# Performance work log

Measured on AMD Instinct MI355X. Metric: run time of the kernel, lower is better.

## Reference

```python
import jax, jax.numpy as jnp
import numpy as np

B, CIN, CE, CA, N, S = 2, 64, 128, 128, 1024, 32
SCALE = np.sqrt(np.float32(CA))  # scale_mode == 'dimfts'


def _vnlin(W, x):
    # VNLinear: linear map over the channel dim of (B, C, 3, N, S)
    return jnp.einsum('oc,bcdns->bodns', W, x)


def setup_inputs() -> dict:
    key = jax.random.key(0)
    ks = jax.random.split(key, 16)
    def w(k, o, i):
        return (jax.random.normal(k, (o, i), jnp.float32) / np.sqrt(np.float32(i)))
    return {
        'group_xyz': jax.random.normal(ks[0], (B, N, S, 3), jnp.float32),
        'group_fts': jax.random.normal(ks[1], (B, CIN, 3, N, S), jnp.float32),
        'query_xyz': jax.random.normal(ks[2], (B, N, 3), jnp.float32),
        'W_e1': w(ks[3], CE, CIN), 'W_e2': w(ks[4], CE, CE),
        'W_q': w(ks[5], CA, CE), 'W_k': w(ks[6], CA, CE), 'W_v': w(ks[7], CA, CE),
        'W_r1': w(ks[8], 64, 1), 'W_r2': w(ks[9], CA, 64),
        'W_std': w(ks[10], 3, CA),
        'W_f1': w(ks[11], CA, CA * 3), 'b_f1': jax.random.normal(ks[12], (CA,), jnp.float32) * 0.02,
        'W_f2': w(ks[13], CA, CA), 'b_f2': jax.random.normal(ks[14], (CA,), jnp.float32) * 0.02,
    }


def reference(group_xyz, group_fts, query_xyz, W_e1, W_e2, W_q, W_k, W_v,
              W_r1, W_r2, W_std, W_f1, b_f1, W_f2, b_f2):
    # vnn_e: two stacked VNLinear layers
    group_emb = _vnlin(W_e2, _vnlin(W_e1, group_fts))        # (B, CE, 3, N, S)
    query_emb = group_emb[..., :1]                           # (B, CE, 3, N, 1)
    q = _vnlin(W_q, query_emb)                               # (B, CA, 3, N, 1)
    k = _vnlin(W_k, group_emb)                               # (B, CA, 3, N, S)
    v = _vnlin(W_v, group_emb)                               # (B, CA, 3, N, S)

    # positional relation: xyz_rel -> (B, 1, 3, N, S) -> vnn_r
    xyz_rel = group_xyz - query_xyz[:, :, None, :]           # (B, N, S, 3)
    xyz_rel = jnp.transpose(xyz_rel[:, :, :, None, :], (0, 3, 4, 1, 2))  # (B,1,3,N,S)
    pos_rel = _vnlin(W_r2, _vnlin(W_r1, xyz_rel))            # (B, CA, 3, N, S)

    # relation_func == 'sub'
    attn = q - k + pos_rel                                   # (B, CA, 3, N, S)

    # VNStdFeatureLin (dim=5, no frame normalization): z0 = VNLinear(CA->3)
    z0 = _vnlin(W_std, attn)                                 # (B, 3, 3, N, S)
    attn = jnp.einsum('bijns,bjkns->bikns', attn, z0)        # (B, CA, 3, N, S) invariant

    # attn_fwd: 1x1 conv -> ReLU -> 1x1 conv on (B, CA*3, N, S)
    attn = attn.reshape(B, CA * 3, N, S)
    h = jax.nn.relu(jnp.einsum('oc,bcns->bons', W_f1, attn) + b_f1[:, None, None])
    a = jnp.einsum('oc,bcns->bons', W_f2, h) + b_f2[:, None, None]  # (B, CA, N, S)

    a = jax.nn.softmax(a[:, :, None, :, :] / SCALE, axis=-1)  # (B, CA, 1, N, S)
    v = v + pos_rel
    resi = jnp.sum(a * v, axis=-1)                            # (B, CA, 3, N)
    return resi
```

## Files before the change

kernel.cpp:

```cpp
#include <hip/hip_runtime.h>
#include <hip/hip_bf16.h>
#include <math.h>

typedef __hip_bfloat16  bf16;
typedef __hip_bfloat162 bf162;
typedef __attribute__((ext_vector_type(8))) short short8;
typedef __attribute__((ext_vector_type(4))) float f32x4;

#define BB   2
#define CINC 64
#define NN   1024
#define SSS  32
#define NS   (NN * SSS)

#define OFF_WE21 0
#define OFF_WR   8192
#define OFF_KBA  8320
#define OFF_VB   16512
#define OFF_F1B  20608
#define OFF_F2B  45184
#define WS_NEED_FLOATS 53376

#define S_ATT_B  0
#define S_FTS_B  26112
#define S_SCR_B  26112
#define S_XYZ_B  30720
#define SMEM_BYTES 30912

__device__ __forceinline__ float bf2f(short s) {
    unsigned int u = ((unsigned int)(unsigned short)s) << 16;
    return __uint_as_float(u);
}
__device__ __forceinline__ short f2bf(float f) {
    bf16 h = __float2bfloat16(f);
    return *reinterpret_cast<short*>(&h);
}
__device__ __forceinline__ unsigned pk2(float a, float b) {
    bf162 p = __float22bfloat162_rn(make_float2(a, b));
    return *reinterpret_cast<unsigned*>(&p);
}

__global__ __launch_bounds__(256) void prep1(const float* __restrict__ We1,
                                             const float* __restrict__ We2,
                                             float* __restrict__ ws) {
    int e = blockIdx.x * 256 + threadIdx.x;
    int o = e >> 6, c = e & 63;
    float acc = 0.f;
    for (int m = 0; m < 128; ++m)
        acc = fmaf(We2[o * 128 + m], We1[m * 64 + c], acc);
    ws[OFF_WE21 + o * 64 + c] = acc;
}

__global__ __launch_bounds__(256) void prep2(const float* __restrict__ Wq,
                                             const float* __restrict__ Wk,
                                             const float* __restrict__ Wv,
                                             const float* __restrict__ Wr1,
                                             const float* __restrict__ Wr2,
                                             const float* __restrict__ Wf1,
                                             const float* __restrict__ Wf2,
                                             float* __restrict__ ws) {
    const float* we21 = ws + OFF_WE21;
    int e = blockIdx.x * 256 + threadIdx.x;
    if (e < 16384) {
        int i = e >> 7, c2 = e & 127;
        const float* W = (c2 < 64) ? Wk : Wq;
        int c = c2 & 63;
        float acc = 0.f;
        for (int o = 0; o < 128; ++o)
            acc = fmaf(W[i * 128 + o], we21[o * 64 + c], acc);
        if (c2 >= 64) acc = -acc;
        ((bf16*)(ws + OFF_KBA))[i * 128 + c2] = __float2bfloat16(acc);
    } else if (e < 24576) {
        int le = e - 16384;
        int i = le >> 6, c = le & 63;
        float acc = 0.f;
        for (int o = 0; o < 128; ++o)
            acc = fmaf(Wv[i * 128 + o], we21[o * 64 + c], acc);
        ((bf16*)(ws + OFF_VB))[i * 64 + c] = __float2bfloat16(acc);
    } else if (e < 24704) {
        int i = e - 24576;
        float acc = 0.f;
        for (int m = 0; m < 64; ++m)
            acc = fmaf(Wr2[i * 64 + m], Wr1[m], acc);
        ws[OFF_WR + i] = acc;
    } else if (e < 24704 + 49152) {
        int f = e - 24704;
        int o = f / 384, kp = f - o * 384;
        int c = (kp & 127) * 3 + (kp >> 7);
        ((bf16*)(ws + OFF_F1B))[f] = __float2bfloat16(Wf1[o * 384 + c]);
    } else if (e < 24704 + 49152 + 16384) {
        int f = e - (24704 + 49152);
        ((bf16*)(ws + OFF_F2B))[f] = __float2bfloat16(Wf2[f]);
    }
}

__global__ __launch_bounds__(256, 2) void fused_main(
        const float* __restrict__ gxyz, const float* __restrict__ gfts,
        const float* __restrict__ qxyz, const float* __restrict__ Wstd,
        const float* __restrict__ bf1,  const float* __restrict__ bf2,
        const float* __restrict__ ws,   float* __restrict__ out) {
    extern __shared__ char smc[];
    short* s_att  = (short*)(smc + S_ATT_B);
    short* h_t    = s_att;
    short* a_t    = s_att + 4352;
    short* fts_s  = (short*)(smc + S_FTS_B);
    float* s_scr  = (float*)(smc + S_SCR_B);
    short* s_xyzh = (short*)(smc + S_XYZ_B);

    const int t    = threadIdx.x;
    const int bid  = blockIdx.x;
    const int b    = bid >> 10;
    const int n    = bid & 1023;
    const int w    = t >> 6;
    const int lane = t & 63;
    const int quad = lane >> 4;
    const int lq   = lane & 15;
    const int wb   = 32 * w;

    const float* gb = gfts + (size_t)b * (CINC * 3 * NS) + n * SSS;

    short8 Ka[2][4], Va[2][2];
    {
        const short* kba = (const short*)(ws + OFF_KBA);
        const short* vbb = (const short*)(ws + OFF_VB);
        #pragma unroll
        for (int it = 0; it < 2; ++it) {
            int i = wb + it * 16 + lq;
            #pragma unroll
            for (int kc = 0; kc < 4; ++kc)
                Ka[it][kc] = *(const short8*)(kba + i * 128 + kc * 32 + quad * 8);
            #pragma unroll
            for (int kc = 0; kc < 2; ++kc)
                Va[it][kc] = *(const short8*)(vbb + i * 64 + kc * 32 + quad * 8);
        }
    }
    float wr2[2] = { ws[OFF_WR + wb + lq], ws[OFF_WR + wb + 16 + lq] };

    uint2 va_pk[6][2];
    #pragma unroll
    for (int h = 0; h < 3; ++h) {
        {
            int cp = t >> 3;
            int ml = (t & 7) * 4;
            const float* fb = gb + (2 * cp * 3 + h) * NS + ml;
            float4 f0 = *(const float4*)(fb);
            float4 f1 = *(const float4*)(fb + 3 * NS);
            short* dst = fts_s + ml * 72 + 2 * cp;
            *(unsigned*)(dst)       = pk2(f0.x, f1.x);
            *(unsigned*)(dst + 72)  = pk2(f0.y, f1.y);
            *(unsigned*)(dst + 144) = pk2(f0.z, f1.z);
            *(unsigned*)(dst + 216) = pk2(f0.w, f1.w);
        }
        if (h == 0 && t >= 160) {
            int id = t - 160;
            int d = id >> 5, s = id & 31;
            s_xyzh[id] = f2bf(gxyz[((b * NN + n) * SSS + s) * 3 + d]
                              - qxyz[(b * NN + n) * 3 + d]);
        }
        __syncthreads();

        const short* qp = fts_s + quad * 8;
        short8 aq0 = *(const short8*)(qp);
        short8 aq1 = *(const short8*)(qp + 32);
        #pragma unroll
        for (int mt_h = 0; mt_h < 2; ++mt_h) {
            int mt = h * 2 + mt_h;
            const short* ap = fts_s + (mt_h * 16 + lq) * 72 + quad * 8;
            short8 a0 = *(const short8*)(ap);
            short8 a1 = *(const short8*)(ap + 32);
            #pragma unroll
            for (int it = 0; it < 2; ++it) {
                f32x4 kk = {0.f, 0.f, 0.f, 0.f};
                kk = __builtin_amdgcn_mfma_f32_16x16x32_bf16(a0,  Ka[it][0], kk, 0, 0, 0);
                kk = __builtin_amdgcn_mfma_f32_16x16x32_bf16(a1,  Ka[it][1], kk, 0, 0, 0);
                kk = __builtin_amdgcn_mfma_f32_16x16x32_bf16(aq0, Ka[it][2], kk, 0, 0, 0);
                kk = __builtin_amdgcn_mfma_f32_16x16x32_bf16(aq1, Ka[it][3], kk, 0, 0, 0);
                f32x4 vv = {0.f, 0.f, 0.f, 0.f};
                vv = __builtin_amdgcn_mfma_f32_16x16x32_bf16(a0,  Va[it][0], vv, 0, 0, 0);
                vv = __builtin_amdgcn_mfma_f32_16x16x32_bf16(a1,  Va[it][1], vv, 0, 0, 0);
                int i = wb + it * 16 + lq;
                float p[4];
                #pragma unroll
                for (int reg = 0; reg < 4; ++reg) {
                    int m = mt * 16 + quad * 4 + reg;
                    float pos = wr2[it] * bf2f(s_xyzh[m]);
                    s_att[m * 136 + i] = f2bf(pos - kk[reg]);
                    p[reg] = vv[reg] + pos;
                }
                va_pk[mt][it].x = pk2(p[0], p[1]);
                va_pk[mt][it].y = pk2(p[2], p[3]);
            }
        }
        __syncthreads();
    }

    {
        short8 As[4];
        #pragma unroll
        for (int kc = 0; kc < 4; ++kc) {
            short8 a = {0, 0, 0, 0, 0, 0, 0, 0};
            if (lq < 3) {
                const float* wp = Wstd + lq * 128 + kc * 32 + quad * 8;
                float4 w0 = *(const float4*)(wp);
                float4 w1 = *(const float4*)(wp + 4);
                a[0] = f2bf(w0.x); a[1] = f2bf(w0.y); a[2] = f2bf(w0.z); a[3] = f2bf(w0.w);
                a[4] = f2bf(w1.x); a[5] = f2bf(w1.y); a[6] = f2bf(w1.z); a[7] = f2bf(w1.w);
            }
            As[kc] = a;
        }
        for (int tile = w; tile < 6; tile += 4) {
            f32x4 acc = {0.f, 0.f, 0.f, 0.f};
            const short* bp = s_att + (tile * 16 + lq) * 136 + quad * 8;
            #pragma unroll
            for (int kc = 0; kc < 4; ++kc) {
                short8 bfr = *(const short8*)(bp + kc * 32);
                acc = __builtin_amdgcn_mfma_f32_16x16x32_bf16(As[kc], bfr, acc, 0, 0, 0);
            }
            if (quad == 0) {
                #pragma unroll
                for (int reg = 0; reg < 3; ++reg)
                    s_scr[reg * 96 + tile * 16 + lq] = acc[reg];
            }
        }
    }
    __syncthreads();

    for (int u = t; u < 512; u += 256) {
        int s  = u >> 4;
        int i0 = (u & 15) * 8;
        float z[3][3];
        #pragma unroll
        for (int j = 0; j < 3; ++j)
            #pragma unroll
            for (int kk = 0; kk < 3; ++kk)
                z[j][kk] = s_scr[j * 96 + kk * 32 + s];
        float af[3][8];
        #pragma unroll
        for (int j = 0; j < 3; ++j) {
            short8 v8 = *(const short8*)(s_att + (j * 32 + s) * 136 + i0);
            #pragma unroll
            for (int x = 0; x < 8; ++x) af[j][x] = bf2f(v8[x]);
        }
        #pragma unroll
        for (int kk = 0; kk < 3; ++kk) {
            short8 o8;
            #pragma unroll
            for (int x = 0; x < 8; ++x)
                o8[x] = f2bf(af[0][x] * z[0][kk] + af[1][x] * z[1][kk] + af[2][x] * z[2][kk]);
            *(short8*)(s_att + (kk * 32 + s) * 136 + i0) = o8;
        }
    }
    __syncthreads();

    f32x4 eacc[2][2];
    {
        f32x4 zz = {0.f, 0.f, 0.f, 0.f};
        eacc[0][0] = zz; eacc[0][1] = zz; eacc[1][0] = zz; eacc[1][1] = zz;
        const short* f1b = (const short*)(ws + OFF_F1B);
        const short* ab0 = f1b + (wb + lq) * 384 + quad * 8;
        const short* ab1 = ab0 + 16 * 384;
        #pragma unroll 2
        for (int ks = 0; ks < 12; ++ks) {
            int kk = ks >> 2;
            int ic = (ks & 3) * 32 + quad * 8;
            short8 a0 = *(const short8*)(ab0 + ks * 32);
            short8 a1 = *(const short8*)(ab1 + ks * 32);
            const short* bp = s_att + (kk * 32) * 136 + ic;
            short8 b0 = *(const short8*)(bp + lq * 136);
            short8 b1 = *(const short8*)(bp + (lq + 16) * 136);
            eacc[0][0] = __builtin_amdgcn_mfma_f32_16x16x32_bf16(a0, b0, eacc[0][0], 0, 0, 0);
            eacc[0][1] = __builtin_amdgcn_mfma_f32_16x16x32_bf16(a0, b1, eacc[0][1], 0, 0, 0);
            eacc[1][0] = __builtin_amdgcn_mfma_f32_16x16x32_bf16(a1, b0, eacc[1][0], 0, 0, 0);
            eacc[1][1] = __builtin_amdgcn_mfma_f32_16x16x32_bf16(a1, b1, eacc[1][1], 0, 0, 0);
        }
    }
    __syncthreads();

    #pragma unroll
    for (int mt = 0; mt < 2; ++mt) {
        int ob = wb + mt * 16 + quad * 4;
        float4 bb = *(const float4*)(bf1 + ob);
        float bv[4] = {bb.x, bb.y, bb.z, bb.w};
        #pragma unroll
        for (int nt = 0; nt < 2; ++nt) {
            f32x4 c = eacc[mt][nt];
            int s = nt * 16 + lq;
            uint2 pk;
            pk.x = pk2(fmaxf(c[0] + bv[0], 0.f), fmaxf(c[1] + bv[1], 0.f));
            pk.y = pk2(fmaxf(c[2] + bv[2], 0.f), fmaxf(c[3] + bv[3], 0.f));
            *(uint2*)(h_t + s * 136 + ob) = pk;
        }
    }
    __syncthreads();

    {
        f32x4 facc[2][2];
        f32x4 zz = {0.f, 0.f, 0.f, 0.f};
        facc[0][0] = zz; facc[0][1] = zz; facc[1][0] = zz; facc[1][1] = zz;
        const short* f2b = (const short*)(ws + OFF_F2B);
        const short* ab0 = f2b + (wb + lq) * 128 + quad * 8;
        const short* ab1 = ab0 + 16 * 128;
        #pragma unroll 2
        for (int ks = 0; ks < 4; ++ks) {
            int c0 = ks * 32 + quad * 8;
            short8 a0 = *(const short8*)(ab0 + ks * 32);
            short8 a1 = *(const short8*)(ab1 + ks * 32);
            short8 b0 = *(const short8*)(h_t + lq * 136 + c0);
            short8 b1 = *(const short8*)(h_t + (lq + 16) * 136 + c0);
            facc[0][0] = __builtin_amdgcn_mfma_f32_16x16x32_bf16(a0, b0, facc[0][0], 0, 0, 0);
            facc[0][1] = __builtin_amdgcn_mfma_f32_16x16x32_bf16(a0, b1, facc[0][1], 0, 0, 0);
            facc[1][0] = __builtin_amdgcn_mfma_f32_16x16x32_bf16(a1, b0, facc[1][0], 0, 0, 0);
            facc[1][1] = __builtin_amdgcn_mfma_f32_16x16x32_bf16(a1, b1, facc[1][1], 0, 0, 0);
        }
        const float inv = 0.08838834764831845f;
        #pragma unroll
        for (int mt = 0; mt < 2; ++mt) {
            int ob = wb + mt * 16 + quad * 4;
            float4 bb = *(const float4*)(bf2 + ob);
            float bv[4] = {bb.x, bb.y, bb.z, bb.w};
            float a0v[4], a1v[4];
            #pragma unroll
            for (int reg = 0; reg < 4; ++reg) {
                float v0 = facc[mt][0][reg] + bv[reg];
                float v1 = facc[mt][1][reg] + bv[reg];
                float mx = fmaxf(v0, v1);
                mx = fmaxf(mx, __shfl_xor(mx, 1));
                mx = fmaxf(mx, __shfl_xor(mx, 2));
                mx = fmaxf(mx, __shfl_xor(mx, 4));
                mx = fmaxf(mx, __shfl_xor(mx, 8));
                float e0 = __expf((v0 - mx) * inv);
                float e1 = __expf((v1 - mx) * inv);
                float sm = e0 + e1;
                sm += __shfl_xor(sm, 1);
                sm += __shfl_xor(sm, 2);
                sm += __shfl_xor(sm, 4);
                sm += __shfl_xor(sm, 8);
                float rs = 1.f / sm;
                a0v[reg] = e0 * rs;
                a1v[reg] = e1 * rs;
            }
            uint2 pk;
            pk.x = pk2(a0v[0], a0v[1]);
            pk.y = pk2(a0v[2], a0v[3]);
            *(uint2*)(a_t + lq * 136 + ob) = pk;
            pk.x = pk2(a1v[0], a1v[1]);
            pk.y = pk2(a1v[2], a1v[3]);
            *(uint2*)(a_t + (16 + lq) * 136 + ob) = pk;
        }
    }
    __syncthreads();

    {
        float pr[2][3];
        #pragma unroll
        for (int it = 0; it < 2; ++it)
            #pragma unroll
            for (int d = 0; d < 3; ++d) pr[it][d] = 0.f;
        #pragma unroll
        for (int mt = 0; mt < 6; ++mt) {
            int d = mt >> 1;
            int s0 = (mt & 1) * 16 + quad * 4;
            #pragma unroll
            for (int it = 0; it < 2; ++it) {
                int i = wb + it * 16 + lq;
                uint2 vp = va_pk[mt][it];
                float v0 = bf2f((short)(vp.x & 0xffff));
                float v1 = bf2f((short)(vp.x >> 16));
                float v2 = bf2f((short)(vp.y & 0xffff));
                float v3 = bf2f((short)(vp.y >> 16));
                pr[it][d] = fmaf(bf2f(a_t[(s0 + 0) * 136 + i]), v0, pr[it][d]);
                pr[it][d] = fmaf(bf2f(a_t[(s0 + 1) * 136 + i]), v1, pr[it][d]);
                pr[it][d] = fmaf(bf2f(a_t[(s0 + 2) * 136 + i]), v2, pr[it][d]);
                pr[it][d] = fmaf(bf2f(a_t[(s0 + 3) * 136 + i]), v3, pr[it][d]);
            }
        }
        #pragma unroll
        for (int it = 0; it < 2; ++it)
            #pragma unroll
            for (int d = 0; d < 3; ++d) {
                float v = pr[it][d];
                v += __shfl_xor(v, 16);
                v += __shfl_xor(v, 32);
                if (quad == 0) s_scr[(wb + it * 16 + lq) * 3 + d] = v;
            }
    }
    __syncthreads();

    for (int e = t; e < 384; e += 256)
        out[(b * 384 + e) * NN + n] = s_scr[e];
}

extern "C" void kernel_launch(void* const* d_in, const int* in_sizes, int n_in,
                              void* d_out, int out_size, void* d_ws, size_t ws_size,
                              hipStream_t stream) {
    const float* gxyz = (const float*)d_in[0];
    const float* gfts = (const float*)d_in[1];
    const float* qxyz = (const float*)d_in[2];
    const float* We1  = (const float*)d_in[3];
    const float* We2  = (const float*)d_in[4];
    const float* Wq   = (const float*)d_in[5];
    const float* Wk   = (const float*)d_in[6];
    const float* Wv   = (const float*)d_in[7];
    const float* Wr1  = (const float*)d_in[8];
    const float* Wr2  = (const float*)d_in[9];
    const float* Wstd = (const float*)d_in[10];
    const float* bf1  = (const float*)d_in[12];
    const float* bf2  = (const float*)d_in[14];
    float* out = (float*)d_out;
    float* ws  = (float*)d_ws;

    (void)hipFuncSetAttribute((const void*)fused_main,
                              hipFuncAttributeMaxDynamicSharedMemorySize, SMEM_BYTES);

    prep1<<<32, 256, 0, stream>>>(We1, We2, ws);
    prep2<<<353, 256, 0, stream>>>(Wq, Wk, Wv, Wr1, Wr2,
                                   (const float*)d_in[11], (const float*)d_in[13], ws);
    fused_main<<<BB * NN, 256, SMEM_BYTES, stream>>>(gxyz, gfts, qxyz, Wstd,
                                                     bf1, bf2, ws, out);
}
```

Before: 184.8 us.

## Process two query points per 512-thread block with vectorized paired output stores

```diff
diff --git a/kernel.cpp b/kernel.cpp
--- a/kernel.cpp
+++ b/kernel.cpp
@@ -21,11 +21,12 @@
 #define OFF_F2B  45184
 #define WS_NEED_FLOATS 53376
 
-#define S_ATT_B  0
-#define S_FTS_B  26112
-#define S_SCR_B  26112
-#define S_XYZ_B  30720
-#define SMEM_BYTES 30912
+#define S_ATT_NL 26112
+#define S_FTS_B  52224
+#define S_FTS_NL 4608
+#define S_XYZ_B  61440
+#define S_XYZ_NL 192
+#define SMEM_BYTES 61824
 
 __device__ __forceinline__ float bf2f(short s) {
     unsigned int u = ((unsigned int)(unsigned short)s) << 16;
@@ -94,25 +95,28 @@
     }
 }
 
-__global__ __launch_bounds__(256, 2) void fused_main(
+__global__ __launch_bounds__(512, 4) void fused_main(
         const float* __restrict__ gxyz, const float* __restrict__ gfts,
         const float* __restrict__ qxyz, const float* __restrict__ Wstd,
         const float* __restrict__ bf1,  const float* __restrict__ bf2,
         const float* __restrict__ ws,   float* __restrict__ out) {
     extern __shared__ char smc[];
-    short* s_att  = (short*)(smc + S_ATT_B);
+    const int t    = threadIdx.x;
+    const int nl   = t >> 8;
+    const int tl   = t & 255;
+    short* s_att  = (short*)(smc + nl * S_ATT_NL);
     short* h_t    = s_att;
     short* a_t    = s_att + 4352;
-    short* fts_s  = (short*)(smc + S_FTS_B);
-    float* s_scr  = (float*)(smc + S_SCR_B);
-    short* s_xyzh = (short*)(smc + S_XYZ_B);
-
-    const int t    = threadIdx.x;
+    short* fts_s  = (short*)(smc + S_FTS_B + nl * S_FTS_NL);
+    float* s_scr  = (float*)(smc + S_FTS_B + nl * S_FTS_NL);
+    short* s_xyzh = (short*)(smc + S_XYZ_B + nl * S_XYZ_NL);
+
     const int bid  = blockIdx.x;
-    const int b    = bid >> 10;
-    const int n    = bid & 1023;
-    const int w    = t >> 6;
-    const int lane = t & 63;
+    const int b    = bid >> 9;
+    const int n0   = (bid & 511) << 1;
+    const int n    = n0 | nl;
+    const int w    = tl >> 6;
+    const int lane = tl & 63;
     const int quad = lane >> 4;
     const int lq   = lane & 15;
     const int wb   = 32 * w;
@@ -140,8 +144,8 @@
     #pragma unroll
     for (int h = 0; h < 3; ++h) {
         {
-            int cp = t >> 3;
-            int ml = (t & 7) * 4;
+            int cp = tl >> 3;
+            int ml = (tl & 7) * 4;
             const float* fb = gb + (2 * cp * 3 + h) * NS + ml;
             float4 f0 = *(const float4*)(fb);
             float4 f1 = *(const float4*)(fb + 3 * NS);
@@ -151,8 +155,8 @@
             *(unsigned*)(dst + 144) = pk2(f0.z, f1.z);
             *(unsigned*)(dst + 216) = pk2(f0.w, f1.w);
         }
-        if (h == 0 && t >= 160) {
-            int id = t - 160;
+        if (h == 0 && tl >= 160) {
+            int id = tl - 160;
             int d = id >> 5, s = id & 31;
             s_xyzh[id] = f2bf(gxyz[((b * NN + n) * SSS + s) * 3 + d]
                               - qxyz[(b * NN + n) * 3 + d]);
@@ -225,7 +229,7 @@
     }
     __syncthreads();
 
-    for (int u = t; u < 512; u += 256) {
+    for (int u = tl; u < 512; u += 256) {
         int s  = u >> 4;
         int i0 = (u & 15) * 8;
         float z[3][3];
@@ -386,8 +390,12 @@
     }
     __syncthreads();
 
-    for (int e = t; e < 384; e += 256)
-        out[(b * 384 + e) * NN + n] = s_scr[e];
+    if (t < 384) {
+        const float* scr0 = (const float*)(smc + S_FTS_B);
+        const float* scr1 = (const float*)(smc + S_FTS_B + S_FTS_NL);
+        float2 o2 = make_float2(scr0[t], scr1[t]);
+        *(float2*)(out + (size_t)(b * 384 + t) * NN + n0) = o2;
+    }
 }
 
 extern "C" void kernel_launch(void* const* d_in, const int* in_sizes, int n_in,
@@ -415,6 +423,6 @@
     prep1<<<32, 256, 0, stream>>>(We1, We2, ws);
     prep2<<<353, 256, 0, stream>>>(Wq, Wk, Wv, Wr1, Wr2,
                                    (const float*)d_in[11], (const float*)d_in[13], ws);
-    fused_main<<<BB * NN, 256, SMEM_BYTES, stream>>>(gxyz, gfts, qxyz, Wstd,
-                                                     bf1, bf2, ws, out);
-}
+    fused_main<<<BB * NN / 2, 512, SMEM_BYTES, stream>>>(gxyz, gfts, qxyz, Wstd,
+                                                         bf1, bf2, ws, out);
+}
```

Measured after the change: 203.3 us. 1.1x slower.
